# Performance work log

Measured on AMD Instinct MI355X. Metric: run time of the kernel, lower is better.

The kernel has to match this reference:

```python
import jax, jax.numpy as jnp
import numpy as np

RES = (32, 32, 32)   # S, H, W
WS = 4               # window size (cubic)
SHIFT = 2            # shift size
NH = 6               # num heads
C = 192              # dim
EPS = 1e-5


def _rel_pos_index(ws):
    coords = np.stack(np.meshgrid(np.arange(ws), np.arange(ws), np.arange(ws), indexing='ij'))
    cf = coords.reshape(3, -1)                      # (3, N)
    rc = (cf[:, :, None] - cf[:, None, :]).transpose(1, 2, 0).astype(np.int64)  # (N,N,3)
    rc[..., 0] += ws - 1
    rc[..., 1] += ws - 1
    rc[..., 2] += ws - 1
    rc[..., 0] *= 3 * ws - 1
    rc[..., 1] *= 2 * ws - 1
    return rc.sum(-1)                               # (N, N)

_RPI = jnp.asarray(_rel_pos_index(WS))


def _ln(x, g, b):
    m = jnp.mean(x, axis=-1, keepdims=True)
    v = jnp.mean(jnp.square(x - m), axis=-1, keepdims=True)
    return (x - m) * jax.lax.rsqrt(v + EPS) * g + b


def setup_inputs():
    key = jax.random.key(0)
    ks = jax.random.split(key, 12)
    B, L = 2, RES[0] * RES[1] * RES[2]
    nW, N = 512, WS ** 3
    Hd = 4 * C
    p = lambda k, s: jax.random.normal(k, s, jnp.float32) * 0.02
    return {
        'x': jax.random.normal(ks[0], (B, L, C), jnp.float32),
        'mask_matrix': jax.random.normal(ks[1], (nW, N, N), jnp.float32),
        'skip': jax.random.normal(ks[2], (B, L, C), jnp.float32),
        'x_up': jax.random.normal(ks[3], (B, L, C), jnp.float32),
        'norm1_g': jnp.ones((C,), jnp.float32), 'norm1_b': jnp.zeros((C,), jnp.float32),
        'kv_w': p(ks[4], (C, 2 * C)), 'kv_b': jnp.zeros((2 * C,), jnp.float32),
        'rpb_table': p(ks[5], ((2 * WS - 1) ** 3, NH)),
        'proj_w': p(ks[6], (C, C)), 'proj_b': jnp.zeros((C,), jnp.float32),
        'norm2_g': jnp.ones((C,), jnp.float32), 'norm2_b': jnp.zeros((C,), jnp.float32),
        'fc1_w': p(ks[7], (C, Hd)), 'fc1_b': jnp.zeros((Hd,), jnp.float32),
        'fc2_w': p(ks[8], (Hd, C)), 'fc2_b': jnp.zeros((C,), jnp.float32),
    }


def reference(x, mask_matrix, skip, x_up, norm1_g, norm1_b, kv_w, kv_b, rpb_table,
              proj_w, proj_b, norm2_g, norm2_b, fc1_w, fc1_b, fc2_w, fc2_b):
    B, L, _ = x.shape
    S, H, W = RES
    ws, N = WS, WS ** 3
    hd = C // NH
    scale = hd ** -0.5

    sn = _ln(skip, norm1_g, norm1_b).reshape(B, S, H, W, C)
    qn = _ln(x_up, norm1_g, norm1_b).reshape(B, S, H, W, C)
    # cyclic shift (shift_size > 0)
    sn = jnp.roll(sn, (-SHIFT, -SHIFT, -SHIFT), axis=(1, 2, 3))
    qn = jnp.roll(qn, (-SHIFT, -SHIFT, -SHIFT), axis=(1, 2, 3))

    def part(t):  # window partition -> (B*nW, N, C)
        t = t.reshape(B, S // ws, ws, H // ws, ws, W // ws, ws, C)
        return t.transpose(0, 1, 3, 5, 2, 4, 6, 7).reshape(-1, N, C)

    skw, qw = part(sn), part(qn)
    B_ = skw.shape[0]

    kv = (skw @ kv_w + kv_b).reshape(B_, N, 2, NH, hd)
    k = kv[:, :, 0].transpose(0, 2, 1, 3)   # (B_, NH, N, hd)
    v = kv[:, :, 1].transpose(0, 2, 1, 3)
    q = qw.reshape(B_, N, NH, hd).transpose(0, 2, 1, 3) * scale

    attn = jnp.einsum('bhqd,bhkd->bhqk', q, k)
    rpb = rpb_table[_RPI.reshape(-1)].reshape(N, N, NH).transpose(2, 0, 1)  # (NH, N, N)
    attn = attn + rpb[None]
    nW = mask_matrix.shape[0]
    attn = attn.reshape(B, nW, NH, N, N) + mask_matrix[None, :, None]
    attn = jax.nn.softmax(attn.reshape(B_, NH, N, N), axis=-1)

    out = jnp.einsum('bhqk,bhkd->bhqd', attn, v).transpose(0, 2, 1, 3).reshape(B_, N, C)
    out = out @ proj_w + proj_b

    # window reverse
    out = out.reshape(B, S // ws, H // ws, W // ws, ws, ws, ws, C)
    out = out.transpose(0, 1, 4, 2, 5, 3, 6, 7).reshape(B, S, H, W, C)
    out = jnp.roll(out, (SHIFT, SHIFT, SHIFT), axis=(1, 2, 3)).reshape(B, L, C)

    x = x + out
    h = _ln(x, norm2_g, norm2_b)
    h = jax.nn.gelu(h @ fc1_w + fc1_b, approximate=False) @ fc2_w + fc2_b
    return x + h
```

## Files before the change

### kernel.cpp

```cpp
#include <hip/hip_runtime.h>
#include <math.h>

typedef unsigned short u16;
typedef __bf16 bf16x8 __attribute__((ext_vector_type(8)));
typedef float f32x4 __attribute__((ext_vector_type(4)));
typedef unsigned short u16x8 __attribute__((ext_vector_type(8)));

#define SHIFT 2

static __device__ __forceinline__ f32x4 mfma16(bf16x8 a, bf16x8 b, f32x4 c) {
  return __builtin_amdgcn_mfma_f32_16x16x32_bf16(a, b, c, 0, 0, 0);
}
static __device__ __forceinline__ u16 f2bf(float f) {
  unsigned u = __builtin_bit_cast(unsigned, f);
  unsigned r = u + 0x7fffu + ((u >> 16) & 1u);
  return (u16)(r >> 16);
}
static __device__ __forceinline__ float bf2f(u16 u) {
  unsigned v = (unsigned)u << 16;
  return __builtin_bit_cast(float, v);
}
static __device__ __forceinline__ void stage16(const u16* g, u16* lbase, int lane) {
#if __has_builtin(__builtin_amdgcn_global_load_lds)
  __builtin_amdgcn_global_load_lds(
      (const __attribute__((address_space(1))) unsigned int*)g,
      (__attribute__((address_space(3))) unsigned int*)lbase, 16, 0, 0);
#else
  *(u16x8*)(lbase + lane * 8) = *(const u16x8*)g;
#endif
}

#define OFF_KVWT  ((size_t)0)
#define OFF_PRWT  (OFF_KVWT + 384*192*2)
#define OFF_FC1WT (OFF_PRWT + 192*192*2)
#define OFF_FC2WT (OFF_FC1WT + 768*192*2)
#define OFF_SKW   (OFF_FC2WT + 192*768*2)
#define OFF_QW    (OFF_SKW + (size_t)65536*192*2)
#define OFF_KVB   (OFF_QW + (size_t)65536*192*2)
#define OFF_POX   (OFF_KVB + (size_t)65536*384*2)
#define OFF_YB    (OFF_POX + (size_t)65536*192*2)
#define OFF_RPBG  (OFF_YB + (size_t)65536*192*2)

__global__ __launch_bounds__(256) void k_prep(
    const float* __restrict__ kv_w, const float* __restrict__ proj_w,
    const float* __restrict__ fc1_w, const float* __restrict__ fc2_w,
    const float* __restrict__ rpb,
    u16* __restrict__ kvT, u16* __restrict__ prT,
    u16* __restrict__ f1T, u16* __restrict__ f2T, u16* __restrict__ rpbg) {
  int i = blockIdx.x * 256 + threadIdx.x;
  if (i < 192 * 384) kvT[(i % 384) * 192 + i / 384] = f2bf(kv_w[i]);
  if (i < 192 * 192) prT[(i % 192) * 192 + i / 192] = f2bf(proj_w[i]);
  if (i < 192 * 768) f1T[(i % 768) * 192 + i / 768] = f2bf(fc1_w[i]);
  if (i < 768 * 192) f2T[(i % 192) * 768 + i / 192] = f2bf(fc2_w[i]);
  if (i < 24576) {
    int h = i >> 12, rem = i & 4095, qr = rem >> 6, kc = rem & 63;
    int qs = qr >> 4, qh = (qr >> 2) & 3, qx = qr & 3;
    int ks = kc >> 4, kh = (kc >> 2) & 3, kx = kc & 3;
    int idx = (qs - ks + 3) * 11 + (qh - kh + 3) * 7 + (qx - kx + 3);
    rpbg[i] = f2bf(rpb[idx * 6 + h]);
  }
}

__global__ __launch_bounds__(256) void k_ln_part(
    const float* __restrict__ skip, const float* __restrict__ x_up,
    const float* __restrict__ gam, const float* __restrict__ bet,
    u16* __restrict__ skw, u16* __restrict__ qw) {
  int row = blockIdx.x * 4 + (threadIdx.x >> 6);
  int lane = threadIdx.x & 63;
  const float* sp = skip + (size_t)row * 192;
  const float* qp = x_up + (size_t)row * 192;
  float sv[3], qv[3], ss = 0.f, qs = 0.f;
#pragma unroll
  for (int j = 0; j < 3; j++) {
    sv[j] = sp[lane + 64 * j]; qv[j] = qp[lane + 64 * j];
    ss += sv[j]; qs += qv[j];
  }
#pragma unroll
  for (int m = 1; m < 64; m <<= 1) { ss += __shfl_xor(ss, m, 64); qs += __shfl_xor(qs, m, 64); }
  float sm = ss * (1.f / 192.f), qm = qs * (1.f / 192.f);
  float s2 = 0.f, q2 = 0.f;
#pragma unroll
  for (int j = 0; j < 3; j++) { float d = sv[j] - sm; s2 += d * d; d = qv[j] - qm; q2 += d * d; }
#pragma unroll
  for (int m = 1; m < 64; m <<= 1) { s2 += __shfl_xor(s2, m, 64); q2 += __shfl_xor(q2, m, 64); }
  float sr = rsqrtf(s2 * (1.f / 192.f) + 1e-5f), qr = rsqrtf(q2 * (1.f / 192.f) + 1e-5f);
  int b = row >> 15, l = row & 32767;
  int s = l >> 10, h = (l >> 5) & 31, w = l & 31;
  int s_ = (s - SHIFT) & 31, h_ = (h - SHIFT) & 31, w_ = (w - SHIFT) & 31;
  int wIdx = ((s_ >> 2) * 8 + (h_ >> 2)) * 8 + (w_ >> 2);
  int n = ((s_ & 3) * 4 + (h_ & 3)) * 4 + (w_ & 3);
  size_t orow = ((size_t)(b * 512 + wIdx) * 64 + n) * 192;
  const float scale = 0.17677669529663687f;
#pragma unroll
  for (int j = 0; j < 3; j++) {
    int cc = lane + 64 * j;
    float gg = gam[cc], bb = bet[cc];
    skw[orow + cc] = f2bf((sv[j] - sm) * sr * gg + bb);
    qw[orow + cc]  = f2bf(((qv[j] - qm) * qr * gg + bb) * scale);
  }
}

__global__ __launch_bounds__(256, 2) void k_kv(
    const u16* __restrict__ A, const u16* __restrict__ BT,
    const float* __restrict__ bias, u16* __restrict__ outh) {
  __shared__ u16 lw[192 * 192];
  int mb = blockIdx.x, nb = blockIdx.y;
  int tid = threadIdx.x, l = tid & 63, wv = tid >> 6, g = l >> 4, c = l & 15;
  int wr = wv >> 1, wc = wv & 1;
#pragma unroll
  for (int i = 0; i < 18; i++) {
    int CI = i * 256 + tid;
    int row = CI / 24, ch = CI % 24;
    int sch = (ch & 24) | ((ch ^ row) & 7);
    stage16(BT + (size_t)(nb * 192 + row) * 192 + sch * 8, lw + (i * 256 + wv * 64) * 8, l);
  }
  __syncthreads();
  f32x4 acc[4][6] = {};
#pragma unroll
  for (int ks = 0; ks < 6; ks++) {
    bf16x8 a[4];
#pragma unroll
    for (int m = 0; m < 4; m++)
      a[m] = *(const bf16x8*)&A[(size_t)(mb * 128 + wr * 64 + m * 16 + c) * 192 + ks * 32 + g * 8];
#pragma unroll
    for (int n = 0; n < 6; n++) {
      int col = wc * 96 + n * 16 + c;
      int ch = ks * 4 + g;
      int chp = (ch & 24) | ((ch ^ col) & 7);
      bf16x8 b = *(const bf16x8*)&lw[col * 192 + chp * 8];
#pragma unroll
      for (int m = 0; m < 4; m++) acc[m][n] = mfma16(a[m], b, acc[m][n]);
    }
  }
#pragma unroll
  for (int n = 0; n < 6; n++)
#pragma unroll
    for (int m = 0; m < 4; m++) {
      int col = nb * 192 + wc * 96 + n * 16 + c;
      float bb = bias[col];
#pragma unroll
      for (int r = 0; r < 4; r++) {
        int row = mb * 128 + wr * 64 + m * 16 + g * 4 + r;
        outh[(size_t)row * 384 + col] = f2bf(acc[m][n][r] + bb);
      }
    }
}

__global__ __launch_bounds__(384) void k_attn_mega(
    const u16* __restrict__ qw, const u16* __restrict__ kvb,
    const u16* __restrict__ rpbg, const float* __restrict__ mask,
    const u16* __restrict__ prT, const float* __restrict__ proj_b,
    u16* __restrict__ pox) {
  __shared__ __align__(16) char smem[38400];
  u16* lv = (u16*)smem;
  u16* lo = (u16*)smem;
  u16* lp = (u16*)(smem + 24576);
  int b_ = blockIdx.x, wIdx = b_ & 511;
  int tid = threadIdx.x, l = tid & 63, wv = tid >> 6, g = l >> 4, c = l & 15;
  int h = wv;
#pragma unroll
  for (int i = 0; i < 4; i++) {
    int CI = i * 384 + tid;
    int row = CI / 24, ch = CI % 24;
    stage16(kvb + ((size_t)b_ * 64 + row) * 384 + 192 + ch * 8,
            lv + (i * 384 + wv * 64) * 8, l);
  }
  const float* mrow = mask + (size_t)wIdx * 4096;
  float4 mv[4][4];
#pragma unroll
  for (int n = 0; n < 4; n++)
#pragma unroll
    for (int m = 0; m < 4; m++)
      mv[n][m] = *(const float4*)&mrow[(n * 16 + c) * 64 + m * 16 + g * 4];
  bf16x8 qa[4], kb[4];
#pragma unroll
  for (int m = 0; m < 4; m++)
    qa[m] = *(const bf16x8*)&qw[((size_t)b_ * 64 + m * 16 + c) * 192 + h * 32 + g * 8];
#pragma unroll
  for (int n = 0; n < 4; n++)
    kb[n] = *(const bf16x8*)&kvb[((size_t)b_ * 64 + n * 16 + c) * 384 + h * 32 + g * 8];
  __syncthreads();
  bf16x8 vb[2][2];
#pragma unroll
  for (int kk = 0; kk < 2; kk++)
#pragma unroll
    for (int nd = 0; nd < 2; nd++) {
      union { u16 u[8]; bf16x8 v; } bb;
#pragma unroll
      for (int j = 0; j < 8; j++)
        bb.u[j] = lv[(kk * 32 + g * 8 + j) * 192 + h * 32 + nd * 16 + c];
      vb[kk][nd] = bb.v;
    }
  __syncthreads();
  f32x4 acc[4][4] = {};
#pragma unroll
  for (int m = 0; m < 4; m++)
#pragma unroll
    for (int n = 0; n < 4; n++) acc[m][n] = mfma16(kb[m], qa[n], acc[m][n]);
  const u16* rg = rpbg + h * 4096;
  f32x4 oacc[4][2] = {};
#pragma unroll
  for (int n = 0; n < 4; n++) {
    ushort4 rv[4];
#pragma unroll
    for (int m = 0; m < 4; m++)
      rv[m] = *(const ushort4*)&rg[(n * 16 + c) * 64 + m * 16 + g * 4];
    float vals[4][4];
    float mx = -3.4e38f;
#pragma unroll
    for (int m = 0; m < 4; m++) {
      float mr[4] = {mv[n][m].x, mv[n][m].y, mv[n][m].z, mv[n][m].w};
      u16 ru[4] = {rv[m].x, rv[m].y, rv[m].z, rv[m].w};
#pragma unroll
      for (int r = 0; r < 4; r++) {
        vals[m][r] = acc[m][n][r] + bf2f(ru[r]) + mr[r];
        mx = fmaxf(mx, vals[m][r]);
      }
    }
    mx = fmaxf(mx, __shfl_xor(mx, 16, 64));
    mx = fmaxf(mx, __shfl_xor(mx, 32, 64));
    float sum = 0.f;
#pragma unroll
    for (int m = 0; m < 4; m++)
#pragma unroll
      for (int r = 0; r < 4; r++) { vals[m][r] = __expf(vals[m][r] - mx); sum += vals[m][r]; }
    sum += __shfl_xor(sum, 16, 64);
    sum += __shfl_xor(sum, 32, 64);
    float inv = 1.f / sum;
#pragma unroll
    for (int m = 0; m < 4; m++) {
      unsigned p0 = f2bf(vals[m][0] * inv) | ((unsigned)f2bf(vals[m][1] * inv) << 16);
      unsigned p1 = f2bf(vals[m][2] * inv) | ((unsigned)f2bf(vals[m][3] * inv) << 16);
      *(uint2*)&lp[h * 1152 + c * 72 + m * 16 + g * 4] = make_uint2(p0, p1);
    }
#pragma unroll
    for (int kk = 0; kk < 2; kk++) {
      bf16x8 pa = *(const bf16x8*)&lp[h * 1152 + c * 72 + kk * 32 + g * 8];
#pragma unroll
      for (int nd = 0; nd < 2; nd++) oacc[n][nd] = mfma16(pa, vb[kk][nd], oacc[n][nd]);
    }
  }
  __syncthreads();
#pragma unroll
  for (int m = 0; m < 4; m++)
#pragma unroll
    for (int nd = 0; nd < 2; nd++)
#pragma unroll
      for (int r = 0; r < 4; r++)
        lo[(m * 16 + g * 4 + r) * 200 + h * 32 + nd * 16 + c] = f2bf(oacc[m][nd][r]);
  __syncthreads();
  f32x4 pacc[4][2] = {};
#pragma unroll
  for (int ks = 0; ks < 6; ks++) {
    bf16x8 pa[4];
#pragma unroll
    for (int m = 0; m < 4; m++)
      pa[m] = *(const bf16x8*)&lo[(m * 16 + c) * 200 + ks * 32 + g * 8];
#pragma unroll
    for (int n = 0; n < 2; n++) {
      bf16x8 pb = *(const bf16x8*)&prT[(size_t)(wv * 32 + n * 16 + c) * 192 + ks * 32 + g * 8];
#pragma unroll
      for (int m = 0; m < 4; m++) pacc[m][n] = mfma16(pa[m], pb, pacc[m][n]);
    }
  }
#pragma unroll
  for (int m = 0; m < 4; m++)
#pragma unroll
    for (int r = 0; r < 4; r++) {
      int tok = m * 16 + g * 4 + r;
#pragma unroll
      for (int n = 0; n < 2; n++) {
        int col = wv * 32 + n * 16 + c;
        pox[((size_t)b_ * 64 + tok) * 192 + col] = f2bf(pacc[m][n][r] + proj_b[col]);
      }
    }
}

__global__ __launch_bounds__(512) void k_mlp(
    const float* __restrict__ x, const u16* __restrict__ pox,
    const float* __restrict__ g2, const float* __restrict__ b2,
    const u16* __restrict__ f1T, const u16* __restrict__ f2T,
    const float* __restrict__ b1, const float* __restrict__ b2f,
    u16* __restrict__ yb, float* __restrict__ out) {
  __shared__ u16 lds[33792];
  u16* f1c = lds;
  u16* f2c = lds + 12288;
  u16* h1c = lds + 24576;
  int tid = threadIdx.x, l = tid & 63, wv = tid >> 6, g = l >> 4, c = l & 15;
  size_t tok0 = (size_t)blockIdx.x * 128 + wv * 16;
  u16* tile = h1c + wv * 1152;
#pragma unroll
  for (int i = 0; i < 3; i++) {
    int CI = i * 512 + tid;
    int row = CI / 24, chs = CI % 24;
    int sch = (chs & 24) | ((chs ^ row) & 7);
    stage16(f1T + (size_t)row * 192 + sch * 8, f1c + (i * 512 + wv * 64) * 8, l);
  }
#pragma unroll
  for (int i = 0; i < 3; i++) {
    int CI = i * 512 + tid;
    int row = CI >> 3, chs = CI & 7;
    int sch = chs ^ (row & 7);
    stage16(f2T + (size_t)row * 768 + sch * 8, f2c + (i * 512 + wv * 64) * 8, l);
  }
  int t = (int)tok0 + c;
  int bI = t >> 15, llt = t & 32767;
  int s = llt >> 10, hh = (llt >> 5) & 31, w = llt & 31;
  int s_ = (s - SHIFT) & 31, h_ = (hh - SHIFT) & 31, w_ = (w - SHIFT) & 31;
  int wI = ((s_ >> 2) * 8 + (h_ >> 2)) * 8 + (w_ >> 2);
  int nn = ((s_ & 3) * 4 + (h_ & 3)) * 4 + (w_ & 3);
  size_t wrow = ((size_t)(bI * 512 + wI) * 64 + nn) * 192;
  bf16x8 hb[6];
  float ss = 0.f, sq = 0.f;
#pragma unroll
  for (int ks = 0; ks < 6; ks++) {
    int ch0 = ks * 32 + g * 8;
    union { u16x8 p; u16 u[8]; } pk;
    pk.p = *(const u16x8*)&pox[wrow + ch0];
    float4 xa = *(const float4*)&x[(size_t)t * 192 + ch0];
    float4 xb = *(const float4*)&x[(size_t)t * 192 + ch0 + 4];
    float y[8] = {xa.x, xa.y, xa.z, xa.w, xb.x, xb.y, xb.z, xb.w};
    union { u16 u[8]; u16x8 v; bf16x8 bv; } yy;
#pragma unroll
    for (int j = 0; j < 8; j++) {
      y[j] += bf2f(pk.u[j]);
      ss += y[j]; sq += y[j] * y[j];
      yy.u[j] = f2bf(y[j]);
    }
    *(u16x8*)&yb[(size_t)t * 192 + ch0] = yy.v;
    hb[ks] = yy.bv;
  }
  ss += __shfl_xor(ss, 16, 64); ss += __shfl_xor(ss, 32, 64);
  sq += __shfl_xor(sq, 16, 64); sq += __shfl_xor(sq, 32, 64);
  {
    float mu = ss * (1.f / 192.f);
    float rs = rsqrtf(sq * (1.f / 192.f) - mu * mu + 1e-5f);
#pragma unroll
    for (int ks = 0; ks < 6; ks++) {
      int ch0 = ks * 32 + g * 8;
      float4 ga = *(const float4*)&g2[ch0];
      float4 gb = *(const float4*)&g2[ch0 + 4];
      float4 ba = *(const float4*)&b2[ch0];
      float4 bb = *(const float4*)&b2[ch0 + 4];
      float gv[8] = {ga.x, ga.y, ga.z, ga.w, gb.x, gb.y, gb.z, gb.w};
      float bv[8] = {ba.x, ba.y, ba.z, ba.w, bb.x, bb.y, bb.z, bb.w};
      union { u16x8 v; u16 u[8]; bf16x8 bvv; } yy, hn_;
      yy.bvv = hb[ks];
#pragma unroll
      for (int j = 0; j < 8; j++)
        hn_.u[j] = f2bf((bf2f(yy.u[j]) - mu) * rs * gv[j] + bv[j]);
      hb[ks] = hn_.bvv;
    }
  }
  __syncthreads();
  f32x4 acc2[12] = {};
#pragma unroll 1
  for (int ko = 0; ko < 12; ko++) {
    f32x4 acc1[4] = {};
#pragma unroll
    for (int ks = 0; ks < 6; ks++) {
      int ch = ks * 4 + g;
      int chp = (ch & 24) | ((ch ^ c) & 7);
#pragma unroll
      for (int cf = 0; cf < 4; cf++) {
        bf16x8 wa = *(const bf16x8*)&f1c[(cf * 16 + c) * 192 + chp * 8];
        acc1[cf] = mfma16(wa, hb[ks], acc1[cf]);
      }
    }
#pragma unroll
    for (int cf = 0; cf < 4; cf++) {
      float4 b1v = *(const float4*)&b1[ko * 64 + cf * 16 + g * 4];
      unsigned pk[2];
#pragma unroll
      for (int p = 0; p < 2; p++) {
        unsigned lohi[2];
#pragma unroll
        for (int q = 0; q < 2; q++) {
          int r = p * 2 + q;
          float v = acc1[cf][r] + (r == 0 ? b1v.x : r == 1 ? b1v.y : r == 2 ? b1v.z : b1v.w);
          float u2 = v * (1.5957691216f + 0.0713548163f * v * v);
          v = v * (1.f / (1.f + __expf(-u2)));
          lohi[q] = f2bf(v);
        }
        pk[p] = lohi[0] | (lohi[1] << 16);
      }
      *(uint2*)&tile[c * 72 + cf * 16 + g * 4] = make_uint2(pk[0], pk[1]);
    }
    __syncthreads();
    if (ko < 11) {
#pragma unroll
      for (int i = 0; i < 3; i++) {
        int CI = i * 512 + tid;
        int row = CI / 24, chs = CI % 24;
        int sch = (chs & 24) | ((chs ^ row) & 7);
        stage16(f1T + (size_t)((ko + 1) * 64 + row) * 192 + sch * 8,
                f1c + (i * 512 + wv * 64) * 8, l);
      }
    }
#pragma unroll
    for (int ck = 0; ck < 2; ck++) {
      bf16x8 a2 = *(const bf16x8*)&tile[c * 72 + ck * 32 + g * 8];
      int ch = ck * 4 + g;
      int chp = ch ^ (c & 7);
#pragma unroll
      for (int of = 0; of < 12; of++) {
        bf16x8 wb = *(const bf16x8*)&f2c[(of * 16 + c) * 64 + chp * 8];
        acc2[of] = mfma16(a2, wb, acc2[of]);
      }
    }
    __syncthreads();
    if (ko < 11) {
#pragma unroll
      for (int i = 0; i < 3; i++) {
        int CI = i * 512 + tid;
        int row = CI >> 3, chs = CI & 7;
        int sch = chs ^ (row & 7);
        stage16(f2T + (size_t)row * 768 + (ko + 1) * 64 + sch * 8,
                f2c + (i * 512 + wv * 64) * 8, l);
      }
    }
  }
#pragma unroll
  for (int of = 0; of < 12; of++) {
    int col = of * 16 + c;
    float bb = b2f[col];
#pragma unroll
    for (int r = 0; r < 4; r++) {
      size_t trow = tok0 + g * 4 + r;
      size_t base = trow * 192 + col;
      out[base] = acc2[of][r] + bb + bf2f(yb[base]);
    }
  }
}

extern "C" void kernel_launch(void* const* d_in, const int* in_sizes, int n_in,
                              void* d_out, int out_size, void* d_ws, size_t ws_size,
                              hipStream_t stream) {
  const float* x      = (const float*)d_in[0];
  const float* mask   = (const float*)d_in[1];
  const float* skip   = (const float*)d_in[2];
  const float* x_up   = (const float*)d_in[3];
  const float* n1g    = (const float*)d_in[4];
  const float* n1b    = (const float*)d_in[5];
  const float* kv_w   = (const float*)d_in[6];
  const float* kv_b   = (const float*)d_in[7];
  const float* rpb    = (const float*)d_in[8];
  const float* proj_w = (const float*)d_in[9];
  const float* proj_b = (const float*)d_in[10];
  const float* n2g    = (const float*)d_in[11];
  const float* n2b    = (const float*)d_in[12];
  const float* fc1_w  = (const float*)d_in[13];
  const float* fc1_b  = (const float*)d_in[14];
  const float* fc2_w  = (const float*)d_in[15];
  const float* fc2_b  = (const float*)d_in[16];
  char* ws = (char*)d_ws;
  u16* kvT  = (u16*)(ws + OFF_KVWT);
  u16* prT  = (u16*)(ws + OFF_PRWT);
  u16* f1T  = (u16*)(ws + OFF_FC1WT);
  u16* f2T  = (u16*)(ws + OFF_FC2WT);
  u16* skw  = (u16*)(ws + OFF_SKW);
  u16* qw   = (u16*)(ws + OFF_QW);
  u16* kvb  = (u16*)(ws + OFF_KVB);
  u16* pox  = (u16*)(ws + OFF_POX);
  u16* yb   = (u16*)(ws + OFF_YB);
  u16* rpbg = (u16*)(ws + OFF_RPBG);
  float* out = (float*)d_out;

  k_prep<<<dim3(576), dim3(256), 0, stream>>>(kv_w, proj_w, fc1_w, fc2_w, rpb,
                                              kvT, prT, f1T, f2T, rpbg);
  k_ln_part<<<dim3(16384), dim3(256), 0, stream>>>(skip, x_up, n1g, n1b, skw, qw);
  k_kv<<<dim3(512, 2), dim3(256), 0, stream>>>(skw, kvT, kv_b, kvb);
  k_attn_mega<<<dim3(1024), dim3(384), 0, stream>>>(
      qw, kvb, rpbg, mask, prT, proj_b, pox);
  k_mlp<<<dim3(512), dim3(512), 0, stream>>>(
      x, pox, n2g, n2b, f1T, f2T, fc1_b, fc2_b, yb, out);
}
```

Before: 221.8 us.

## Process two token tiles per wave in MLP kernel to reuse weight fragments

```diff
diff --git a/kernel.cpp b/kernel.cpp
--- a/kernel.cpp
+++ b/kernel.cpp
@@ -276,7 +276,7 @@
     }
 }
 
-__global__ __launch_bounds__(512) void k_mlp(
+__global__ __launch_bounds__(256) void k_mlp(
     const float* __restrict__ x, const u16* __restrict__ pox,
     const float* __restrict__ g2, const float* __restrict__ b2,
     const u16* __restrict__ f1T, const u16* __restrict__ f2T,
@@ -287,52 +287,54 @@
   u16* f2c = lds + 12288;
   u16* h1c = lds + 24576;
   int tid = threadIdx.x, l = tid & 63, wv = tid >> 6, g = l >> 4, c = l & 15;
-  size_t tok0 = (size_t)blockIdx.x * 128 + wv * 16;
-  u16* tile = h1c + wv * 1152;
-#pragma unroll
-  for (int i = 0; i < 3; i++) {
-    int CI = i * 512 + tid;
-    int row = CI / 24, chs = CI % 24;
-    int sch = (chs & 24) | ((chs ^ row) & 7);
-    stage16(f1T + (size_t)row * 192 + sch * 8, f1c + (i * 512 + wv * 64) * 8, l);
-  }
-#pragma unroll
-  for (int i = 0; i < 3; i++) {
-    int CI = i * 512 + tid;
-    int row = CI >> 3, chs = CI & 7;
-    int sch = chs ^ (row & 7);
-    stage16(f2T + (size_t)row * 768 + sch * 8, f2c + (i * 512 + wv * 64) * 8, l);
-  }
-  int t = (int)tok0 + c;
-  int bI = t >> 15, llt = t & 32767;
-  int s = llt >> 10, hh = (llt >> 5) & 31, w = llt & 31;
-  int s_ = (s - SHIFT) & 31, h_ = (hh - SHIFT) & 31, w_ = (w - SHIFT) & 31;
-  int wI = ((s_ >> 2) * 8 + (h_ >> 2)) * 8 + (w_ >> 2);
-  int nn = ((s_ & 3) * 4 + (h_ & 3)) * 4 + (w_ & 3);
-  size_t wrow = ((size_t)(bI * 512 + wI) * 64 + nn) * 192;
-  bf16x8 hb[6];
-  float ss = 0.f, sq = 0.f;
-#pragma unroll
-  for (int ks = 0; ks < 6; ks++) {
-    int ch0 = ks * 32 + g * 8;
-    union { u16x8 p; u16 u[8]; } pk;
-    pk.p = *(const u16x8*)&pox[wrow + ch0];
-    float4 xa = *(const float4*)&x[(size_t)t * 192 + ch0];
-    float4 xb = *(const float4*)&x[(size_t)t * 192 + ch0 + 4];
-    float y[8] = {xa.x, xa.y, xa.z, xa.w, xb.x, xb.y, xb.z, xb.w};
-    union { u16 u[8]; u16x8 v; bf16x8 bv; } yy;
-#pragma unroll
-    for (int j = 0; j < 8; j++) {
-      y[j] += bf2f(pk.u[j]);
-      ss += y[j]; sq += y[j] * y[j];
-      yy.u[j] = f2bf(y[j]);
-    }
-    *(u16x8*)&yb[(size_t)t * 192 + ch0] = yy.v;
-    hb[ks] = yy.bv;
-  }
-  ss += __shfl_xor(ss, 16, 64); ss += __shfl_xor(ss, 32, 64);
-  sq += __shfl_xor(sq, 16, 64); sq += __shfl_xor(sq, 32, 64);
-  {
+  size_t tok0 = (size_t)blockIdx.x * 128 + wv * 32;
+  u16* tile = h1c + wv * 2304;
+  int o1[6], o2[6];
+#pragma unroll
+  for (int i = 0; i < 6; i++) {
+    int CI = i * 256 + tid;
+    int r1 = CI / 24, c1 = CI % 24;
+    o1[i] = r1 * 192 + ((c1 & 24) | ((c1 ^ r1) & 7)) * 8;
+    int r2 = CI >> 3, c2 = CI & 7;
+    o2[i] = r2 * 768 + (c2 ^ (r2 & 7)) * 8;
+  }
+#pragma unroll
+  for (int i = 0; i < 6; i++)
+    stage16(f1T + o1[i], f1c + (i * 256 + wv * 64) * 8, l);
+#pragma unroll
+  for (int i = 0; i < 6; i++)
+    stage16(f2T + o2[i], f2c + (i * 256 + wv * 64) * 8, l);
+  bf16x8 hb[2][6];
+#pragma unroll
+  for (int th = 0; th < 2; th++) {
+    int t = (int)tok0 + th * 16 + c;
+    int bI = t >> 15, llt = t & 32767;
+    int s = llt >> 10, hh = (llt >> 5) & 31, w = llt & 31;
+    int s_ = (s - SHIFT) & 31, h_ = (hh - SHIFT) & 31, w_ = (w - SHIFT) & 31;
+    int wI = ((s_ >> 2) * 8 + (h_ >> 2)) * 8 + (w_ >> 2);
+    int nn = ((s_ & 3) * 4 + (h_ & 3)) * 4 + (w_ & 3);
+    size_t wrow = ((size_t)(bI * 512 + wI) * 64 + nn) * 192;
+    float ss = 0.f, sq = 0.f;
+#pragma unroll
+    for (int ks = 0; ks < 6; ks++) {
+      int ch0 = ks * 32 + g * 8;
+      union { u16x8 p; u16 u[8]; } pk;
+      pk.p = *(const u16x8*)&pox[wrow + ch0];
+      float4 xa = *(const float4*)&x[(size_t)t * 192 + ch0];
+      float4 xb = *(const float4*)&x[(size_t)t * 192 + ch0 + 4];
+      float y[8] = {xa.x, xa.y, xa.z, xa.w, xb.x, xb.y, xb.z, xb.w};
+      union { u16 u[8]; u16x8 v; bf16x8 bv; } yy;
+#pragma unroll
+      for (int j = 0; j < 8; j++) {
+        y[j] += bf2f(pk.u[j]);
+        ss += y[j]; sq += y[j] * y[j];
+        yy.u[j] = f2bf(y[j]);
+      }
+      *(u16x8*)&yb[(size_t)t * 192 + ch0] = yy.v;
+      hb[th][ks] = yy.bv;
+    }
+    ss += __shfl_xor(ss, 16, 64); ss += __shfl_xor(ss, 32, 64);
+    sq += __shfl_xor(sq, 16, 64); sq += __shfl_xor(sq, 32, 64);
     float mu = ss * (1.f / 192.f);
     float rs = rsqrtf(sq * (1.f / 192.f) - mu * mu + 1e-5f);
 #pragma unroll
@@ -345,18 +347,18 @@
       float gv[8] = {ga.x, ga.y, ga.z, ga.w, gb.x, gb.y, gb.z, gb.w};
       float bv[8] = {ba.x, ba.y, ba.z, ba.w, bb.x, bb.y, bb.z, bb.w};
       union { u16x8 v; u16 u[8]; bf16x8 bvv; } yy, hn_;
-      yy.bvv = hb[ks];
+      yy.bvv = hb[th][ks];
 #pragma unroll
       for (int j = 0; j < 8; j++)
         hn_.u[j] = f2bf((bf2f(yy.u[j]) - mu) * rs * gv[j] + bv[j]);
-      hb[ks] = hn_.bvv;
-    }
-  }
-  __syncthreads();
-  f32x4 acc2[12] = {};
+      hb[th][ks] = hn_.bvv;
+    }
+  }
+  __syncthreads();
+  f32x4 acc2[12][2] = {};
 #pragma unroll 1
   for (int ko = 0; ko < 12; ko++) {
-    f32x4 acc1[4] = {};
+    f32x4 acc1[2][4] = {};
 #pragma unroll
     for (int ks = 0; ks < 6; ks++) {
       int ch = ks * 4 + g;
@@ -364,60 +366,61 @@
 #pragma unroll
       for (int cf = 0; cf < 4; cf++) {
         bf16x8 wa = *(const bf16x8*)&f1c[(cf * 16 + c) * 192 + chp * 8];
-        acc1[cf] = mfma16(wa, hb[ks], acc1[cf]);
-      }
-    }
-#pragma unroll
-    for (int cf = 0; cf < 4; cf++) {
-      float4 b1v = *(const float4*)&b1[ko * 64 + cf * 16 + g * 4];
-      unsigned pk[2];
-#pragma unroll
-      for (int p = 0; p < 2; p++) {
-        unsigned lohi[2];
-#pragma unroll
-        for (int q = 0; q < 2; q++) {
-          int r = p * 2 + q;
-          float v = acc1[cf][r] + (r == 0 ? b1v.x : r == 1 ? b1v.y : r == 2 ? b1v.z : b1v.w);
-          float u2 = v * (1.5957691216f + 0.0713548163f * v * v);
-          v = v * (1.f / (1.f + __expf(-u2)));
-          lohi[q] = f2bf(v);
+#pragma unroll
+        for (int th = 0; th < 2; th++)
+          acc1[th][cf] = mfma16(wa, hb[th][ks], acc1[th][cf]);
+      }
+    }
+#pragma unroll
+    for (int th = 0; th < 2; th++)
+#pragma unroll
+      for (int cf = 0; cf < 4; cf++) {
+        float4 b1v = *(const float4*)&b1[ko * 64 + cf * 16 + g * 4];
+        unsigned pk[2];
+#pragma unroll
+        for (int p = 0; p < 2; p++) {
+          unsigned lohi[2];
+#pragma unroll
+          for (int q = 0; q < 2; q++) {
+            int r = p * 2 + q;
+            float v = acc1[th][cf][r] + (r == 0 ? b1v.x : r == 1 ? b1v.y : r == 2 ? b1v.z : b1v.w);
+            float u2 = v * (1.5957691216f + 0.0713548163f * v * v);
+            v = v * (1.f / (1.f + __expf(-u2)));
+            lohi[q] = f2bf(v);
+          }
+          pk[p] = lohi[0] | (lohi[1] << 16);
         }
-        pk[p] = lohi[0] | (lohi[1] << 16);
-      }
-      *(uint2*)&tile[c * 72 + cf * 16 + g * 4] = make_uint2(pk[0], pk[1]);
-    }
+        *(uint2*)&tile[(th * 16 + c) * 72 + cf * 16 + g * 4] = make_uint2(pk[0], pk[1]);
+      }
     __syncthreads();
     if (ko < 11) {
-#pragma unroll
-      for (int i = 0; i < 3; i++) {
-        int CI = i * 512 + tid;
-        int row = CI / 24, chs = CI % 24;
-        int sch = (chs & 24) | ((chs ^ row) & 7);
-        stage16(f1T + (size_t)((ko + 1) * 64 + row) * 192 + sch * 8,
-                f1c + (i * 512 + wv * 64) * 8, l);
-      }
+      const u16* src = f1T + (size_t)(ko + 1) * 12288;
+#pragma unroll
+      for (int i = 0; i < 6; i++)
+        stage16(src + o1[i], f1c + (i * 256 + wv * 64) * 8, l);
     }
 #pragma unroll
     for (int ck = 0; ck < 2; ck++) {
-      bf16x8 a2 = *(const bf16x8*)&tile[c * 72 + ck * 32 + g * 8];
+      bf16x8 a2[2];
+#pragma unroll
+      for (int th = 0; th < 2; th++)
+        a2[th] = *(const bf16x8*)&tile[(th * 16 + c) * 72 + ck * 32 + g * 8];
       int ch = ck * 4 + g;
       int chp = ch ^ (c & 7);
 #pragma unroll
       for (int of = 0; of < 12; of++) {
         bf16x8 wb = *(const bf16x8*)&f2c[(of * 16 + c) * 64 + chp * 8];
-        acc2[of] = mfma16(a2, wb, acc2[of]);
+#pragma unroll
+        for (int th = 0; th < 2; th++)
+          acc2[of][th] = mfma16(a2[th], wb, acc2[of][th]);
       }
     }
     __syncthreads();
     if (ko < 11) {
-#pragma unroll
-      for (int i = 0; i < 3; i++) {
-        int CI = i * 512 + tid;
-        int row = CI >> 3, chs = CI & 7;
-        int sch = chs ^ (row & 7);
-        stage16(f2T + (size_t)row * 768 + (ko + 1) * 64 + sch * 8,
-                f2c + (i * 512 + wv * 64) * 8, l);
-      }
+      const u16* src = f2T + (size_t)(ko + 1) * 64;
+#pragma unroll
+      for (int i = 0; i < 6; i++)
+        stage16(src + o2[i], f2c + (i * 256 + wv * 64) * 8, l);
     }
   }
 #pragma unroll
@@ -425,11 +428,13 @@
     int col = of * 16 + c;
     float bb = b2f[col];
 #pragma unroll
-    for (int r = 0; r < 4; r++) {
-      size_t trow = tok0 + g * 4 + r;
-      size_t base = trow * 192 + col;
-      out[base] = acc2[of][r] + bb + bf2f(yb[base]);
-    }
+    for (int th = 0; th < 2; th++)
+#pragma unroll
+      for (int r = 0; r < 4; r++) {
+        size_t trow = tok0 + th * 16 + g * 4 + r;
+        size_t base = trow * 192 + col;
+        out[base] = acc2[of][th][r] + bb + bf2f(yb[base]);
+      }
   }
 }
 
@@ -472,6 +477,6 @@
   k_kv<<<dim3(512, 2), dim3(256), 0, stream>>>(skw, kvT, kv_b, kvb);
   k_attn_mega<<<dim3(1024), dim3(384), 0, stream>>>(
       qw, kvb, rpbg, mask, prT, proj_b, pox);
-  k_mlp<<<dim3(512), dim3(512), 0, stream>>>(
+  k_mlp<<<dim3(512), dim3(256), 0, stream>>>(
       x, pox, n2g, n2b, f1T, f2T, fc1_b, fc2_b, yb, out);
 }
```

New measurement: 237.2 us. 6.9% more time.
